# Kernel optimization log

Hardware: AMD Instinct MI355X
Metric: run time of the kernel (lower is better)

## Reference

```python
import jax, jax.numpy as jnp
import numpy as np


def _hann(n_fft):
    # torch.hann_window default is periodic: 0.5*(1 - cos(2*pi*n/N))
    n = jnp.arange(n_fft, dtype=jnp.float32)
    return 0.5 * (1.0 - jnp.cos(2.0 * jnp.pi * n / n_fft))


def setup_inputs() -> dict:
    key = jax.random.key(0)
    k1, k2 = jax.random.split(key)
    B, T = 2, 131072
    hop = 256
    n_bins = 257  # n_fft // 2 + 1 with n_fft = 512
    ex = jax.random.normal(k1, (B, T), dtype=jnp.float32)
    log_mag = jax.random.normal(k2, (B, T // hop, n_bins), dtype=jnp.float32) * 0.5
    return {"ex": ex, "log_mag": log_mag, "hop_length": hop}


def reference(ex, log_mag, hop_length):
    # ex: [B, T], log_mag: [B, F, n_fft//2+1]
    B, T = ex.shape
    # zero-phase FIR: irfft of magnitude, then center with fftshift
    mag = jnp.exp(log_mag)
    fir = jnp.fft.irfft(mag, axis=-1)            # [B, F, n_fft]
    n_fft = fir.shape[-1]
    fir = jnp.fft.fftshift(fir, axes=-1)
    kernel = fir * _hann(n_fft)                  # [B, F, n_fft]

    padding = (n_fft - 1) // 2
    padded = jnp.pad(ex, ((0, 0), (padding, padding)))
    win_len = n_fft + hop_length - 1
    n_frames = (padded.shape[1] - win_len) // hop_length + 1
    kernel = kernel[:, :n_frames]                # [B, Fr, n_fft]

    # gather sliding windows: out[b,f,j] = sum_k padded[b, f*hop + j + k] * kernel[b,f,k]
    idx = (jnp.arange(n_frames) * hop_length)[:, None, None] \
        + jnp.arange(hop_length)[None, :, None] \
        + jnp.arange(n_fft)[None, None, :]       # [Fr, hop, n_fft]
    windows = padded[:, idx]                     # [B, Fr, hop, n_fft]
    out = jnp.einsum('bfjk,bfk->bfj', windows, kernel)
    return out.reshape(B, n_frames * hop_length)
```

## Files before the change

kernel.cpp:

```cpp
#include <hip/hip_runtime.h>

#define NFFT    512
#define NBINS   257
#define HOP     256
#define NFRAMES 511
#define TSAMP   131072

__device__ __forceinline__ int SWZ(int i) { return i + ((i >> 5) << 2); }

__global__ __launch_bounds__(256)
void ltv_fir(const float* __restrict__ ex,
             const float* __restrict__ log_mag,
             float* __restrict__ out)
{
    __shared__ float s_mag[NBINS];
    __shared__ float s_de[132];
    __shared__ float s_do[132];
    __shared__ float s_ker[NFFT];
    __shared__ float s_ex[860];
    __shared__ float s_part[8][260];

    const int tid = threadIdx.x;
    const int bf  = blockIdx.x;
    const int b   = bf / NFRAMES;
    const int f   = bf - b * NFRAMES;

    const float* lm = log_mag + ((size_t)b * 512 + f) * NBINS;
    for (int i = tid; i < NBINS; i += 256)
        s_mag[i] = __expf(lm[i]);

    const float* exb = ex + (size_t)b * TSAMP;
    const int base = f * HOP - 255;
    for (int i = tid; i < 768; i += 256) {
        int g = base + i;
        s_ex[SWZ(i)] = (g >= 0 && g < TSAMP) ? exb[g] : 0.0f;
    }
    __syncthreads();

    if (tid < 132) {
        float ve, vo;
        if (tid == 0 || tid >= 129) {
            ve = vo = 0.0f;
        } else if (tid == 128) {
            ve = vo = s_mag[128];
        } else {
            float a = s_mag[tid], c = s_mag[256 - tid];
            float sgn = (tid & 1) ? -1.0f : 1.0f;
            ve = sgn * (a + c);
            vo = sgn * (a - c);
        }
        s_de[tid] = ve;
        s_do[tid] = vo;
    }
    __syncthreads();

    {
        const int wid = tid >> 6;
        const int l   = tid & 63;
        const int par = wid >> 1;
        const int n   = (((wid & 1) << 6) + l) * 2 + par;
        const float theta = 3.14159265358979323846f * (float)n * (1.0f / 256.0f);
        const float t  = cosf(theta);
        const float k2 = 2.0f * t;
        const float* dsel = par ? s_do : s_de;
        float ce = 1.0f;
        float co = t;
        float E = 0.0f, O = 0.0f;
        #pragma unroll 3
        for (int m = 0; m < 132; m += 4) {
            float4 dd = *(const float4*)&dsel[m];
            E = fmaf(dd.x, ce, E);
            O = fmaf(dd.y, co, O);
            float ce2 = fmaf(k2, co,  -ce);
            float co2 = fmaf(k2, ce2, -co);
            E = fmaf(dd.z, ce2, E);
            O = fmaf(dd.w, co2, O);
            ce = fmaf(k2, co2, -ce2);
            co = fmaf(k2, ce,  -co2);
        }
        const float p    = par ? -1.0f : 1.0f;
        const float cst  = s_mag[0] + p * s_mag[256];
        const float inv  = 1.0f / 512.0f;
        const float h_lo = 0.5f * (1.0f - t);
        const float h_hi = 0.5f * (1.0f + t);
        s_ker[n]       = (cst + 2.0f * (E + O)) * h_lo * inv;
        s_ker[n + 256] = (cst + 2.0f * (E - O)) * h_hi * inv;
    }
    __syncthreads();

    {
        const int g   = tid >> 5;
        const int lg  = tid & 31;
        const int kb  = g * 64;
        const int q0i = lg * 8 + kb;
        float acc[8];
        #pragma unroll
        for (int r = 0; r < 8; ++r) acc[r] = 0.0f;
        float w[12];
        *(float4*)&w[0] = *(const float4*)&s_ex[SWZ(q0i)];
        *(float4*)&w[4] = *(const float4*)&s_ex[SWZ(q0i + 4)];
        #pragma unroll
        for (int kc = 0; kc < 64; kc += 4) {
            *(float4*)&w[8] = *(const float4*)&s_ex[SWZ(q0i + kc + 8)];
            float4 kq = *(const float4*)&s_ker[kb + kc];
            #pragma unroll
            for (int r = 0; r < 8; ++r) {
                acc[r] = fmaf(w[r + 0], kq.x, acc[r]);
                acc[r] = fmaf(w[r + 1], kq.y, acc[r]);
                acc[r] = fmaf(w[r + 2], kq.z, acc[r]);
                acc[r] = fmaf(w[r + 3], kq.w, acc[r]);
            }
            #pragma unroll
            for (int i = 0; i < 8; ++i) w[i] = w[i + 4];
        }
        #pragma unroll
        for (int r = 0; r < 8; ++r) s_part[g][lg * 8 + r] = acc[r];
    }
    __syncthreads();

    float r = 0.0f;
    #pragma unroll
    for (int g2 = 0; g2 < 8; ++g2) r += s_part[g2][tid];
    out[((size_t)b * NFRAMES + f) * HOP + tid] = r;
}

extern "C" void kernel_launch(void* const* d_in, const int* in_sizes, int n_in,
                              void* d_out, int out_size, void* d_ws, size_t ws_size,
                              hipStream_t stream)
{
    const float* ex      = (const float*)d_in[0];
    const float* log_mag = (const float*)d_in[1];
    float* out = (float*)d_out;

    dim3 grid(2 * NFRAMES);
    dim3 block(256);
    hipLaunchKernelGGL(ltv_fir, grid, block, 0, stream, ex, log_mag, out);
}
```

Before: 13.35 us.

## Overlap loads with DFT prep, exploit kernel symmetry, retile FIR convolution

Input samples are now loaded as float4 by 192 threads while the other 64 threads compute the exponentiated magnitudes and the even/odd DFT coefficients, which removes one barrier and the separate s_mag staging. The symmetric zero-phase kernel is computed for only 129 cosine indices and mirrored into the other half, cutting the cosine-series work roughly in half. The convolution is retiled so each thread produces 16 outputs over 32 taps, with 16 k-groups and vectorized partial stores. In exchange the partial-sum buffer doubles and per-thread register pressure rises. Only about half the threads are active during the DFT step.

```diff
diff --git a/kernel.cpp b/kernel.cpp
--- a/kernel.cpp
+++ b/kernel.cpp
@@ -13,59 +13,58 @@
              const float* __restrict__ log_mag,
              float* __restrict__ out)
 {
-    __shared__ float s_mag[NBINS];
-    __shared__ float s_de[132];
-    __shared__ float s_do[132];
-    __shared__ float s_ker[NFFT];
-    __shared__ float s_ex[860];
-    __shared__ float s_part[8][260];
+    __shared__ float s_d[2][132];
+    __shared__ float s_c[2];
+    __shared__ float s_ker[512];
+    __shared__ float s_ex[864];
+    __shared__ float s_part[16][260];
 
     const int tid = threadIdx.x;
     const int bf  = blockIdx.x;
     const int b   = bf / NFRAMES;
     const int f   = bf - b * NFRAMES;
 
-    const float* lm = log_mag + ((size_t)b * 512 + f) * NBINS;
-    for (int i = tid; i < NBINS; i += 256)
-        s_mag[i] = __expf(lm[i]);
+    const float* lm  = log_mag + ((size_t)b * 512 + f) * NBINS;
+    const float* exb = ex + (size_t)b * TSAMP;
 
-    const float* exb = ex + (size_t)b * TSAMP;
-    const int base = f * HOP - 255;
-    for (int i = tid; i < 768; i += 256) {
-        int g = base + i;
-        s_ex[SWZ(i)] = (g >= 0 && g < TSAMP) ? exb[g] : 0.0f;
+    if (tid < 192) {
+        const int gw = f * HOP - 256 + tid * 4;
+        float4 q = make_float4(0.f, 0.f, 0.f, 0.f);
+        if (gw >= 0) q = *(const float4*)&exb[gw];
+        const int wb = tid * 4 - 1;
+        if (tid > 0) s_ex[SWZ(wb)] = q.x;
+        s_ex[SWZ(wb + 1)] = q.y;
+        s_ex[SWZ(wb + 2)] = q.z;
+        s_ex[SWZ(wb + 3)] = q.w;
+    } else {
+        #pragma unroll
+        for (int it = 0; it < 3; ++it) {
+            const int s2 = (tid - 192) + 64 * it;
+            if (s2 < 134) {
+                if (s2 == 132)      s_c[0] = __expf(lm[0]);
+                else if (s2 == 133) s_c[1] = __expf(lm[256]);
+                else if (s2 == 0 || s2 >= 129) { s_d[0][s2] = 0.f; s_d[1][s2] = 0.f; }
+                else if (s2 == 128) { const float v = __expf(lm[128]); s_d[0][128] = v; s_d[1][128] = v; }
+                else {
+                    const float a  = __expf(lm[s2]);
+                    const float c0 = __expf(lm[256 - s2]);
+                    const float sg = (s2 & 1) ? -1.f : 1.f;
+                    s_d[0][s2] = sg * (a + c0);
+                    s_d[1][s2] = sg * (a - c0);
+                }
+            }
+        }
     }
     __syncthreads();
 
-    if (tid < 132) {
-        float ve, vo;
-        if (tid == 0 || tid >= 129) {
-            ve = vo = 0.0f;
-        } else if (tid == 128) {
-            ve = vo = s_mag[128];
-        } else {
-            float a = s_mag[tid], c = s_mag[256 - tid];
-            float sgn = (tid & 1) ? -1.0f : 1.0f;
-            ve = sgn * (a + c);
-            vo = sgn * (a - c);
-        }
-        s_de[tid] = ve;
-        s_do[tid] = vo;
-    }
-    __syncthreads();
-
-    {
-        const int wid = tid >> 6;
-        const int l   = tid & 63;
-        const int par = wid >> 1;
-        const int n   = (((wid & 1) << 6) + l) * 2 + par;
-        const float theta = 3.14159265358979323846f * (float)n * (1.0f / 256.0f);
-        const float t  = cosf(theta);
+    if (tid <= 128) {
+        const int wid  = tid >> 6;
+        const int lane = tid & 63;
+        const int n    = (wid == 2) ? 128 : 2 * lane + wid;
+        const float t  = __cosf(3.14159265358979323846f * (float)n * (1.0f / 256.0f));
         const float k2 = 2.0f * t;
-        const float* dsel = par ? s_do : s_de;
-        float ce = 1.0f;
-        float co = t;
-        float E = 0.0f, O = 0.0f;
+        const float* dsel = s_d[n & 1];
+        float ce = 1.0f, co = t, E = 0.0f, O = 0.0f;
         #pragma unroll 3
         for (int m = 0; m < 132; m += 4) {
             float4 dd = *(const float4*)&dsel[m];
@@ -78,49 +77,51 @@
             ce = fmaf(k2, co2, -ce2);
             co = fmaf(k2, ce,  -co2);
         }
-        const float p    = par ? -1.0f : 1.0f;
-        const float cst  = s_mag[0] + p * s_mag[256];
-        const float inv  = 1.0f / 512.0f;
-        const float h_lo = 0.5f * (1.0f - t);
-        const float h_hi = 0.5f * (1.0f + t);
-        s_ker[n]       = (cst + 2.0f * (E + O)) * h_lo * inv;
-        s_ker[n + 256] = (cst + 2.0f * (E - O)) * h_hi * inv;
+        const float p    = (n & 1) ? -1.f : 1.f;
+        const float cst  = s_c[0] + p * s_c[1];
+        const float v_lo = (cst + 2.f * (E + O)) * (0.5f * (1.f - t)) * (1.f / 512.f);
+        const float v_hi = (cst + 2.f * (E - O)) * (0.5f * (1.f + t)) * (1.f / 512.f);
+        s_ker[n]       = v_lo;
+        s_ker[256 - n] = v_hi;
+        if (n > 0) { s_ker[256 + n] = v_hi; s_ker[512 - n] = v_lo; }
     }
     __syncthreads();
 
     {
-        const int g   = tid >> 5;
-        const int lg  = tid & 31;
-        const int kb  = g * 64;
-        const int q0i = lg * 8 + kb;
-        float acc[8];
+        const int g   = tid >> 4;
+        const int lt  = tid & 15;
+        const int kb  = g * 32;
+        const int off = kb + lt * 16;
+        float w[20];
         #pragma unroll
-        for (int r = 0; r < 8; ++r) acc[r] = 0.0f;
-        float w[12];
-        *(float4*)&w[0] = *(const float4*)&s_ex[SWZ(q0i)];
-        *(float4*)&w[4] = *(const float4*)&s_ex[SWZ(q0i + 4)];
+        for (int c = 0; c < 5; ++c)
+            *(float4*)&w[4 * c] = *(const float4*)&s_ex[SWZ(off + 4 * c)];
+        float acc[16];
         #pragma unroll
-        for (int kc = 0; kc < 64; kc += 4) {
-            *(float4*)&w[8] = *(const float4*)&s_ex[SWZ(q0i + kc + 8)];
-            float4 kq = *(const float4*)&s_ker[kb + kc];
+        for (int r = 0; r < 16; ++r) acc[r] = 0.0f;
+        #pragma unroll
+        for (int kc = 0; kc < 32; kc += 4) {
+            const float4 kq = *(const float4*)&s_ker[kb + kc];
             #pragma unroll
-            for (int r = 0; r < 8; ++r) {
-                acc[r] = fmaf(w[r + 0], kq.x, acc[r]);
-                acc[r] = fmaf(w[r + 1], kq.y, acc[r]);
-                acc[r] = fmaf(w[r + 2], kq.z, acc[r]);
-                acc[r] = fmaf(w[r + 3], kq.w, acc[r]);
+            for (int r = 0; r < 16; ++r)
+                acc[r] = fmaf(w[r], kq.x, fmaf(w[r + 1], kq.y,
+                         fmaf(w[r + 2], kq.z, fmaf(w[r + 3], kq.w, acc[r]))));
+            if (kc < 28) {
+                #pragma unroll
+                for (int i = 0; i < 16; ++i) w[i] = w[i + 4];
+                *(float4*)&w[16] = *(const float4*)&s_ex[SWZ(off + kc + 20)];
             }
-            #pragma unroll
-            for (int i = 0; i < 8; ++i) w[i] = w[i + 4];
         }
         #pragma unroll
-        for (int r = 0; r < 8; ++r) s_part[g][lg * 8 + r] = acc[r];
+        for (int c = 0; c < 4; ++c)
+            *(float4*)&s_part[g][lt * 16 + 4 * c] =
+                make_float4(acc[4 * c], acc[4 * c + 1], acc[4 * c + 2], acc[4 * c + 3]);
     }
     __syncthreads();
 
     float r = 0.0f;
     #pragma unroll
-    for (int g2 = 0; g2 < 8; ++g2) r += s_part[g2][tid];
+    for (int gg = 0; gg < 16; ++gg) r += s_part[gg][tid];
     out[((size_t)b * NFRAMES + f) * HOP + tid] = r;
 }
 
```

After: 12.86 us (median of 2 runs). 3.7% less time.
